# Kernel tuning notes

Measured on AMD Instinct MI355X. Metric: run time of the kernel, lower is better.

The kernel has to match this reference:

```python
import jax, jax.numpy as jnp
import numpy as np

D_MODEL = 1024
N_HEAD = 16
D_K = D_MODEL // N_HEAD
B, S = 4, 2048


def setup_inputs() -> dict:
    key = jax.random.key(0)
    ks = jax.random.split(key, 12)
    s = 1.0 / np.sqrt(D_MODEL)
    inp = {
        "q": jax.random.normal(ks[0], (B, S, D_MODEL), jnp.float32),
        "k": jax.random.normal(ks[1], (B, S, D_MODEL), jnp.float32),
        "v": jax.random.normal(ks[2], (B, S, D_MODEL), jnp.float32),
        "mask": jnp.tril(jnp.ones((S, S), dtype=bool)),
        "Wq": jax.random.normal(ks[3], (D_MODEL, D_MODEL), jnp.float32) * s,
        "bq": jnp.zeros((D_MODEL,), jnp.float32),
        "Wk": jax.random.normal(ks[4], (D_MODEL, D_MODEL), jnp.float32) * s,
        "bk": jnp.zeros((D_MODEL,), jnp.float32),
        "Wv": jax.random.normal(ks[5], (D_MODEL, D_MODEL), jnp.float32) * s,
        "bv": jnp.zeros((D_MODEL,), jnp.float32),
        "Wo": jax.random.normal(ks[6], (D_MODEL, D_MODEL), jnp.float32) * s,
        "bo": jnp.zeros((D_MODEL,), jnp.float32),
    }
    return inp


def reference(q, k, v, mask, Wq, bq, Wk, bk, Wv, bv, Wo, bo):
    b, n, d = q.shape
    # NOTE: source module (faithfully) computes the query projection from k.
    qh = (k @ Wq + bq).reshape(b, n, N_HEAD, D_K).transpose(0, 2, 1, 3)  # b h n d_k
    kh = (k @ Wk + bk).reshape(b, n, N_HEAD, D_K).transpose(0, 2, 1, 3)
    vh = (v @ Wv + bv).reshape(b, n, N_HEAD, D_K).transpose(0, 2, 1, 3)
    scores = jnp.einsum("bhqd,bhkd->bhqk", qh, kh) / jnp.sqrt(jnp.float32(D_K))
    scores = jnp.where(mask[None, None, :, :], scores, jnp.float32(-1e9))
    attn = jax.nn.softmax(scores, axis=-1)  # dropout is identity in eval
    out = jnp.einsum("bhqk,bhkd->bhqd", attn, vh)
    out = out.transpose(0, 2, 1, 3).reshape(b, n, d)
    out = out @ Wo + bo  # dropout identity in eval
    return out, attn
```

## Files before the change

kernel.cpp:

```cpp
#include <hip/hip_runtime.h>
#include <hip/hip_bf16.h>

#define S_LEN 2048
#define DMODEL 1024
#define NHEAD 16
#define DK 64
#define BS 4

typedef __attribute__((ext_vector_type(8))) short short8;
typedef __attribute__((ext_vector_type(4))) float f32x4;
typedef __attribute__((ext_vector_type(4))) ushort ushort4v;

__device__ __forceinline__ ushort f2b(float f) {
  __hip_bfloat16 h = __float2bfloat16(f);
  return __builtin_bit_cast(ushort, h);
}

__device__ __forceinline__ void gl_lds16(const void* g, void* l) {
  __builtin_amdgcn_global_load_lds(
      (const __attribute__((address_space(1))) void*)g,
      (__attribute__((address_space(3))) void*)l, 16, 0, 0);
}


__global__ __launch_bounds__(256) void cvt2_kernel(
    const float* __restrict__ a, const float* __restrict__ b,
    ushort* __restrict__ oa, ushort* __restrict__ ob, int n4) {
  int idx = blockIdx.x * 256 + threadIdx.x;
  int stride = gridDim.x * 256;
  for (int i = idx; i < 2 * n4; i += stride) {
    const bool first = (i < n4);
    const int j = first ? i : i - n4;
    f32x4 v = first ? ((const f32x4*)a)[j] : ((const f32x4*)b)[j];
    ushort4v o;
    o[0] = f2b(v[0]); o[1] = f2b(v[1]); o[2] = f2b(v[2]); o[3] = f2b(v[3]);
    if (first) ((ushort4v*)oa)[j] = o; else ((ushort4v*)ob)[j] = o;
  }
}

__global__ __launch_bounds__(256) void transW4_kernel(
    const float* __restrict__ W0, const float* __restrict__ W1,
    const float* __restrict__ W2, const float* __restrict__ W3,
    ushort* __restrict__ T0, ushort* __restrict__ T1,
    ushort* __restrict__ T2, ushort* __restrict__ T3) {
  const float* W;
  ushort* T;
  switch (blockIdx.z) {
    case 0: W = W0; T = T0; break;
    case 1: W = W1; T = T1; break;
    case 2: W = W2; T = T2; break;
    default: W = W3; T = T3; break;
  }
  __shared__ float t[32][33];
  const int n0 = blockIdx.x * 32, k0 = blockIdx.y * 32;
  const int tx = threadIdx.x, ty = threadIdx.y;
#pragma unroll
  for (int i = 0; i < 4; i++)
    t[ty + i * 8][tx] = W[(size_t)(k0 + ty + i * 8) * DMODEL + n0 + tx];
  __syncthreads();
#pragma unroll
  for (int i = 0; i < 4; i++)
    T[(size_t)(n0 + ty + i * 8) * DMODEL + k0 + tx] = f2b(t[tx][ty + i * 8]);
}

template <bool F32OUT, bool QKMODE, bool VT>
__global__ __launch_bounds__(256) void gemm_bt(
    const ushort* __restrict__ A, const ushort* __restrict__ Bt,
    const float* __restrict__ bias, const float* __restrict__ bias1,
    void* __restrict__ Cout, void* __restrict__ Cout1,
    int M, int N, int K) {
  __shared__ ushort Als[128 * 32];
  __shared__ ushort Bls[128 * 32];
  const int tid = threadIdx.x;
  const int lane = tid & 63;
  const int w = tid >> 6;
  const int lo = lane & 15, hi = lane >> 4;
  const int nb = N >> 7;
  const int bm = blockIdx.x / nb, bn = blockIdx.x % nb;
  const int m0 = bm << 7, n0 = bn << 7;
  const int wr = (w >> 1) << 6, wc = (w & 1) << 6;

  f32x4 acc[4][4] = {};

  const int c1 = tid, c2 = tid + 256;
  const int r1 = c1 >> 2, k1 = (c1 & 3) << 3;
  const int r2 = c2 >> 2, k2 = (c2 & 3) << 3;
  const ushort* Ap1 = A + (size_t)(m0 + r1) * K + k1;
  const ushort* Ap2 = A + (size_t)(m0 + r2) * K + k2;
  const ushort* Bp1 = Bt + (size_t)(n0 + r1) * K + k1;
  const ushort* Bp2 = Bt + (size_t)(n0 + r2) * K + k2;
  char* Al = (char*)Als;
  char* Bl = (char*)Bls;

  for (int k0 = 0; k0 < K; k0 += 32) {
    gl_lds16(Ap1 + k0, Al + c1 * 16);
    gl_lds16(Ap2 + k0, Al + c2 * 16);
    gl_lds16(Bp1 + k0, Bl + c1 * 16);
    gl_lds16(Bp2 + k0, Bl + c2 * 16);
    __syncthreads();
    short8 af[4], bf[4];
#pragma unroll
    for (int i = 0; i < 4; i++)
      af[i] = *(const short8*)(Als + (wr + i * 16 + lo) * 32 + hi * 8);
#pragma unroll
    for (int j = 0; j < 4; j++)
      bf[j] = *(const short8*)(Bls + (wc + j * 16 + lo) * 32 + hi * 8);
#pragma unroll
    for (int i = 0; i < 4; i++)
#pragma unroll
      for (int j = 0; j < 4; j++)
        acc[i][j] = __builtin_amdgcn_mfma_f32_16x16x32_bf16(af[i], bf[j], acc[i][j], 0, 0, 0);
    __syncthreads();
  }

#pragma unroll
  for (int j = 0; j < 4; j++) {
    const int col = n0 + wc + j * 16 + lo;
    const float* bp = (QKMODE && col >= 1024) ? bias1 : bias;
    const int colm = QKMODE ? (col & 1023) : col;
    const int cN = QKMODE ? 1024 : N;
    const float bj = bp ? bp[colm] : 0.0f;
    if (VT) {
#pragma unroll
      for (int i = 0; i < 4; i++) {
        const int row0 = m0 + wr + i * 16 + hi * 4;
        ushort4v pk;
#pragma unroll
        for (int r = 0; r < 4; r++) pk[r] = f2b(acc[i][j][r] + bj);
        *(ushort4v*)(&((ushort*)Cout)[(size_t)col * M + row0]) = pk;
      }
    } else {
#pragma unroll
      for (int i = 0; i < 4; i++) {
        const int row0 = m0 + wr + i * 16 + hi * 4;
#pragma unroll
        for (int r = 0; r < 4; r++) {
          float vv = acc[i][j][r] + bj;
          if (F32OUT) {
            __builtin_nontemporal_store(
                vv, &((float*)Cout)[(size_t)(row0 + r) * N + col]);
          } else {
            void* dst = (QKMODE && col >= 1024) ? Cout1 : Cout;
            ((ushort*)dst)[(size_t)(row0 + r) * cN + colm] = f2b(vv);
          }
        }
      }
    }
  }
}

#define SWZ(row) ((((row) & 7) << 5) ^ (((row) & 8) << 1))
__global__ __launch_bounds__(512) void attn_kernel(
    const ushort* __restrict__ Qh, const ushort* __restrict__ Kh,
    const ushort* __restrict__ Vt, float* __restrict__ attn,
    ushort* __restrict__ Ah) {
  const int blk = blockIdx.x;
  const int x = blk & 7;
  const int i2 = blk >> 3;
  const int g = x + ((i2 >> 4) << 3);
  const int tidx = i2 & 15;
  const int t = (tidx & 1) ? (tidx >> 1) : (15 - (tidx >> 1));
  const int h = g & 15;
  const int b = g >> 4;
  const int tid = threadIdx.x;
  const int w = tid >> 6;
  const int lane = tid & 63;
  const int lo = lane & 15, hi = lane >> 4;
  const int q0 = t << 7;
  const int qrow = w * 16 + lo;
  const int qg = q0 + qrow;
  const int tok0 = b * S_LEN + q0 + w * 16;
  const int ktmax = 2 * t + 1;
  const int ntiles = ktmax + 1;

  __shared__ ushort Kls[2][64 * 64];
  __shared__ ushort Vls[2][64 * 64];
  __shared__ float Pf[8][16 * 64];

  short8 aq[2];
  {
    const ushort* qp = Qh + (size_t)(tok0 + lo) * DMODEL + h * DK + hi * 8;
    aq[0] = *(const short8*)qp;
    aq[1] = *(const short8*)(qp + 32);
  }

  const ushort* kbh = Kh + (size_t)(b * S_LEN) * DMODEL + h * DK;
  const ushort* vbh = Vt + (size_t)(h * DK) * (BS * S_LEN) + b * S_LEN;

  const int srow = tid >> 3;
  const int scolb = ((tid & 7) << 4) ^ ((srow & 7) << 4);
  const ushort* ksrc = kbh + (size_t)srow * DMODEL + (scolb >> 1);
  const ushort* vsrc = vbh + (size_t)srow * (BS * S_LEN) + (scolb >> 1);

#define STAGE_K(buf, kt)                                                     \
  gl_lds16(ksrc + (size_t)(kt) * 64 * DMODEL, (char*)&Kls[(buf)][0] + tid * 16)
#define STAGE_V(buf, kt)                                                     \
  gl_lds16(vsrc + (size_t)(kt) * 64, (char*)&Vls[(buf)][0] + tid * 16)

#define QKT(sa, cur)                                                         \
  __builtin_amdgcn_s_setprio(1);                                             \
  _Pragma("unroll") for (int j = 0; j < 4; j++) {                            \
    const int row = j * 16 + lo;                                             \
    short8 b0 = *(const short8*)((const char*)&Kls[(cur)][0] + row * 128 +   \
                                 ((hi * 16) ^ ((row & 7) << 4)));            \
    sa[j] = __builtin_amdgcn_mfma_f32_16x16x32_bf16(b0, aq[0], sa[j], 0, 0, 0); \
  }                                                                          \
  _Pragma("unroll") for (int j = 0; j < 4; j++) {                            \
    const int row = j * 16 + lo;                                             \
    short8 b1 = *(const short8*)((const char*)&Kls[(cur)][0] + row * 128 +   \
                                 ((64 + hi * 16) ^ ((row & 7) << 4)));       \
    sa[j] = __builtin_amdgcn_mfma_f32_16x16x32_bf16(b1, aq[1], sa[j], 0, 0, 0); \
  }                                                                          \
  __builtin_amdgcn_s_setprio(0);

  float* abase =
      attn + (size_t)(b * NHEAD + h) * S_LEN * S_LEN + (size_t)q0 * S_LEN;

  const int zc0 = ntiles << 6;
  const int zcol = zc0 + tid * 4;
  const bool zon = (zcol < S_LEN);
  const f32x4 zv = {0.0f, 0.0f, 0.0f, 0.0f};

  float lsum = 0.0f;
  STAGE_K(0, 0);
  for (int kt = 0; kt <= ktmax; ++kt) {
    const int cur = kt & 1;
    __syncthreads();
    if (kt < ktmax) STAGE_K(cur ^ 1, kt + 1);
    if (zon) {
      const int r0 = (kt * 128) / ntiles;
      const int r1 = ((kt + 1) * 128) / ntiles;
      for (int row = r0; row < r1; ++row)
        __builtin_nontemporal_store(
            zv, (f32x4*)(abase + (size_t)row * S_LEN + zcol));
    }
    f32x4 sa[4] = {};
    QKT(sa, cur)
#pragma unroll
    for (int j = 0; j < 4; j++) {
#pragma unroll
      for (int r = 0; r < 4; r++) {
        const int kg = kt * 64 + j * 16 + hi * 4 + r;
        const float e = __expf(sa[j][r] * 0.125f);
        lsum += (kg > qg) ? 0.0f : e;
      }
    }
  }
  lsum += __shfl_xor(lsum, 16);
  lsum += __shfl_xor(lsum, 32);
  const float invl = 1.0f / lsum;

  f32x4 oacc[4] = {};

  __syncthreads();
  STAGE_K(0, 0);
  STAGE_V(0, 0);
  for (int kt = 0; kt <= ktmax; ++kt) {
    const int cur = kt & 1;
    __syncthreads();
    if (kt < ktmax) { STAGE_K(cur ^ 1, kt + 1); STAGE_V(cur ^ 1, kt + 1); }
    f32x4 sa[4] = {};
    QKT(sa, cur)
#pragma unroll
    for (int j = 0; j < 4; j++) {
      float p[4];
#pragma unroll
      for (int r = 0; r < 4; r++) {
        const int kg = kt * 64 + j * 16 + hi * 4 + r;
        p[r] = (kg > qg) ? 0.0f : __expf(sa[j][r] * 0.125f) * invl;
      }
      f32x4 pv4 = {p[0], p[1], p[2], p[3]};
      *(f32x4*)((char*)&Pf[w][0] + lo * 256 +
                ((j * 64 + hi * 16) ^ SWZ(lo))) = pv4;
    }
#pragma unroll
    for (int t2 = 0; t2 < 4; t2++) {
      const int rr = hi + 4 * t2;
      f32x4 pv = *(const f32x4*)((const char*)&Pf[w][0] + rr * 256 +
                                 ((lo * 16) ^ SWZ(rr)));
      __builtin_nontemporal_store(
          pv,
          (f32x4*)(abase + (size_t)(w * 16 + rr) * S_LEN + kt * 64 + lo * 4));
    }
    short8 ap[2];
#pragma unroll
    for (int ks = 0; ks < 2; ks++) {
      const int base = ks * 128 + hi * 32;
      f32x4 u0 = *(const f32x4*)((const char*)&Pf[w][0] + lo * 256 +
                                 ((base) ^ SWZ(lo)));
      f32x4 u1 = *(const f32x4*)((const char*)&Pf[w][0] + lo * 256 +
                                 ((base + 16) ^ SWZ(lo)));
      short8 a;
      a[0] = f2b(u0[0]); a[1] = f2b(u0[1]); a[2] = f2b(u0[2]); a[3] = f2b(u0[3]);
      a[4] = f2b(u1[0]); a[5] = f2b(u1[1]); a[6] = f2b(u1[2]); a[7] = f2b(u1[3]);
      ap[ks] = a;
    }
    __builtin_amdgcn_s_setprio(1);
#pragma unroll
    for (int dj = 0; dj < 4; dj++) {
      const int row = dj * 16 + lo;
      const char* vrow = (const char*)&Vls[cur][0] + row * 128;
      short8 b0 = *(const short8*)(vrow + ((hi * 16) ^ ((row & 7) << 4)));
      short8 b1 = *(const short8*)(vrow + ((64 + hi * 16) ^ ((row & 7) << 4)));
      oacc[dj] = __builtin_amdgcn_mfma_f32_16x16x32_bf16(ap[0], b0, oacc[dj], 0, 0, 0);
      oacc[dj] = __builtin_amdgcn_mfma_f32_16x16x32_bf16(ap[1], b1, oacc[dj], 0, 0, 0);
    }
    __builtin_amdgcn_s_setprio(0);
  }

#pragma unroll
  for (int dj = 0; dj < 4; dj++)
#pragma unroll
    for (int r = 0; r < 4; r++)
      Ah[(size_t)(tok0 + hi * 4 + r) * DMODEL + h * DK + dj * 16 + lo] =
          f2b(oacc[dj][r]);
#undef STAGE_K
#undef STAGE_V
#undef QKT
}


extern "C" void kernel_launch(void* const* d_in, const int* in_sizes, int n_in,
                              void* d_out, int out_size, void* d_ws,
                              size_t ws_size, hipStream_t stream) {
  const float* kin = (const float*)d_in[1];
  const float* vin = (const float*)d_in[2];
  const float* Wq = (const float*)d_in[4];
  const float* bq = (const float*)d_in[5];
  const float* Wk = (const float*)d_in[6];
  const float* bk = (const float*)d_in[7];
  const float* Wv = (const float*)d_in[8];
  const float* bv = (const float*)d_in[9];
  const float* Wo = (const float*)d_in[10];
  const float* bo = (const float*)d_in[11];

  float* out = (float*)d_out;
  float* attn = out + (size_t)BS * S_LEN * DMODEL;

  char* ws = (char*)d_ws;
  const size_t MB = (size_t)1 << 20;
  ushort* kb   = (ushort*)(ws + 0 * MB);
  ushort* vb   = (ushort*)(ws + 16 * MB);
  ushort* Qh   = (ushort*)(ws + 32 * MB);
  ushort* Kh   = (ushort*)(ws + 48 * MB);
  ushort* Vt   = (ushort*)(ws + 64 * MB);
  ushort* WqkT = (ushort*)(ws + 80 * MB);
  ushort* WvT  = (ushort*)(ws + 84 * MB);
  ushort* WoT  = (ushort*)(ws + 86 * MB);

  const int NTOK4 = (BS * S_LEN * DMODEL) / 4;
  cvt2_kernel<<<4096, 256, 0, stream>>>(kin, vin, kb, vb, NTOK4);

  dim3 tb(32, 8);
  transW4_kernel<<<dim3(32, 32, 4), tb, 0, stream>>>(
      Wq, Wk, Wv, Wo, WqkT, WqkT + (size_t)DMODEL * DMODEL, WvT, WoT);

  gemm_bt<false, true, false><<<64 * 16, 256, 0, stream>>>(
      kb, WqkT, bq, bk, Qh, Kh, 8192, 2048, 1024);
  gemm_bt<false, false, true><<<64 * 8, 256, 0, stream>>>(
      vb, WvT, bv, nullptr, Vt, nullptr, 8192, 1024, 1024);

  ushort* Ahp = kb;
  attn_kernel<<<BS * NHEAD * (S_LEN / 128), 512, 0, stream>>>(Qh, Kh, Vt, attn, Ahp);

  gemm_bt<true, false, false><<<64 * 8, 256, 0, stream>>>(
      Ahp, WoT, bo, nullptr, out, nullptr, 8192, 1024, 1024);
}
```

Baseline: 392.2 us.

## Move causal zero-fill of attention matrix into projection GEMMs and relax barriers

Zeroing of the fully-masked 128x128 upper-triangle tiles of the attention-probability output moves out of the attention kernel and into the Q/K and V projection GEMMs. Each GEMM block writes five such tiles, addressed by a triangular-index decode, once its main loop finishes. The goal is to run this large write stream alongside compute-bound GEMM work instead of inside the attention loop. The second attention pass also replaces its per-iteration __syncthreads with an explicit vmcnt wait plus barrier at the loop end, so prefetch loads can stay in flight. This relies on exact knowledge of outstanding load counts and on the float sqrt-based tile decode being correct.

```diff
diff --git a/kernel.cpp b/kernel.cpp
--- a/kernel.cpp
+++ b/kernel.cpp
@@ -63,12 +63,12 @@
     T[(size_t)(n0 + ty + i * 8) * DMODEL + k0 + tx] = f2b(t[tx][ty + i * 8]);
 }
 
-template <bool F32OUT, bool QKMODE, bool VT>
+template <bool F32OUT, bool QKMODE, bool VT, bool FILL>
 __global__ __launch_bounds__(256) void gemm_bt(
     const ushort* __restrict__ A, const ushort* __restrict__ Bt,
     const float* __restrict__ bias, const float* __restrict__ bias1,
     void* __restrict__ Cout, void* __restrict__ Cout1,
-    int M, int N, int K) {
+    int M, int N, int K, float* __restrict__ fillb, int slab0) {
   __shared__ ushort Als[128 * 32];
   __shared__ ushort Bls[128 * 32];
   const int tid = threadIdx.x;
@@ -111,6 +111,39 @@
       for (int j = 0; j < 4; j++)
         acc[i][j] = __builtin_amdgcn_mfma_f32_16x16x32_bf16(af[i], bf[j], acc[i][j], 0, 0, 0);
     __syncthreads();
+  }
+
+  if (FILL) {
+    const f32x4 zv = {0.0f, 0.0f, 0.0f, 0.0f};
+    const int s0 = slab0 + blockIdx.x * 5;
+    float *fb0, *fb1, *fb2, *fb3, *fb4;
+#define SLAB_BASE(fb, ss)                                                   \
+  {                                                                         \
+    const int s = (ss);                                                     \
+    const int bh = s / 120;                                                 \
+    const int u = s - bh * 120;                                             \
+    const int j = (int)((1.0f + sqrtf(1.0f + 8.0f * (float)u)) * 0.5f);     \
+    const int rb = u - ((j * (j - 1)) >> 1);                                \
+    fb = fillb + (size_t)bh * S_LEN * S_LEN + (size_t)(rb * 128) * S_LEN +  \
+         j * 128;                                                           \
+  }
+    SLAB_BASE(fb0, s0)
+    SLAB_BASE(fb1, s0 + 1)
+    SLAB_BASE(fb2, s0 + 2)
+    SLAB_BASE(fb3, s0 + 3)
+    SLAB_BASE(fb4, s0 + 4)
+#undef SLAB_BASE
+#pragma unroll
+    for (int sl = 0; sl < 5; sl++) {
+      float* bp = (sl == 0) ? fb0 : (sl == 1) ? fb1 : (sl == 2) ? fb2
+                  : (sl == 3) ? fb3 : fb4;
+#pragma unroll
+      for (int q = 0; q < 16; q++) {
+        const int u2 = tid + (q << 8);
+        __builtin_nontemporal_store(
+            zv, (f32x4*)(bp + (size_t)(u2 >> 5) * S_LEN + (u2 & 31) * 4));
+      }
+    }
   }
 
 #pragma unroll
@@ -171,7 +204,6 @@
   const int qg = q0 + qrow;
   const int tok0 = b * S_LEN + q0 + w * 16;
   const int ktmax = 2 * t + 1;
-  const int ntiles = ktmax + 1;
 
   __shared__ ushort Kls[2][64 * 64];
   __shared__ ushort Vls[2][64 * 64];
@@ -216,24 +248,12 @@
   float* abase =
       attn + (size_t)(b * NHEAD + h) * S_LEN * S_LEN + (size_t)q0 * S_LEN;
 
-  const int zc0 = ntiles << 6;
-  const int zcol = zc0 + tid * 4;
-  const bool zon = (zcol < S_LEN);
-  const f32x4 zv = {0.0f, 0.0f, 0.0f, 0.0f};
-
   float lsum = 0.0f;
   STAGE_K(0, 0);
   for (int kt = 0; kt <= ktmax; ++kt) {
     const int cur = kt & 1;
     __syncthreads();
     if (kt < ktmax) STAGE_K(cur ^ 1, kt + 1);
-    if (zon) {
-      const int r0 = (kt * 128) / ntiles;
-      const int r1 = ((kt + 1) * 128) / ntiles;
-      for (int row = r0; row < r1; ++row)
-        __builtin_nontemporal_store(
-            zv, (f32x4*)(abase + (size_t)row * S_LEN + zcol));
-    }
     f32x4 sa[4] = {};
     QKT(sa, cur)
 #pragma unroll
@@ -251,13 +271,11 @@
   const float invl = 1.0f / lsum;
 
   f32x4 oacc[4] = {};
-
-  __syncthreads();
   STAGE_K(0, 0);
   STAGE_V(0, 0);
+  asm volatile("s_waitcnt vmcnt(0)\n\ts_barrier" ::: "memory");
   for (int kt = 0; kt <= ktmax; ++kt) {
     const int cur = kt & 1;
-    __syncthreads();
     if (kt < ktmax) { STAGE_K(cur ^ 1, kt + 1); STAGE_V(cur ^ 1, kt + 1); }
     f32x4 sa[4] = {};
     QKT(sa, cur)
@@ -306,6 +324,7 @@
       oacc[dj] = __builtin_amdgcn_mfma_f32_16x16x32_bf16(ap[1], b1, oacc[dj], 0, 0, 0);
     }
     __builtin_amdgcn_s_setprio(0);
+    asm volatile("s_waitcnt vmcnt(4)\n\ts_barrier" ::: "memory");
   }
 
 #pragma unroll
@@ -355,14 +374,14 @@
   transW4_kernel<<<dim3(32, 32, 4), tb, 0, stream>>>(
       Wq, Wk, Wv, Wo, WqkT, WqkT + (size_t)DMODEL * DMODEL, WvT, WoT);
 
-  gemm_bt<false, true, false><<<64 * 16, 256, 0, stream>>>(
-      kb, WqkT, bq, bk, Qh, Kh, 8192, 2048, 1024);
-  gemm_bt<false, false, true><<<64 * 8, 256, 0, stream>>>(
-      vb, WvT, bv, nullptr, Vt, nullptr, 8192, 1024, 1024);
+  gemm_bt<false, true, false, true><<<64 * 16, 256, 0, stream>>>(
+      kb, WqkT, bq, bk, Qh, Kh, 8192, 2048, 1024, attn, 0);
+  gemm_bt<false, false, true, true><<<64 * 8, 256, 0, stream>>>(
+      vb, WvT, bv, nullptr, Vt, nullptr, 8192, 1024, 1024, attn, 5120);
 
   ushort* Ahp = kb;
   attn_kernel<<<BS * NHEAD * (S_LEN / 128), 512, 0, stream>>>(Qh, Kh, Vt, attn, Ahp);
 
-  gemm_bt<true, false, false><<<64 * 8, 256, 0, stream>>>(
-      Ahp, WoT, bo, nullptr, out, nullptr, 8192, 1024, 1024);
-}
+  gemm_bt<true, false, false, false><<<64 * 8, 256, 0, stream>>>(
+      Ahp, WoT, bo, nullptr, out, nullptr, 8192, 1024, 1024, nullptr, 0);
+}
```

Result: slower. 423.3 us (+7.9%).

## Fuse fp32-to-bf16 activation conversion into projection GEMM A-tile loads

Applied to the files above, without the earlier changes.

Removes the separate conversion kernel that turned k and v into bf16 buffers. The projection GEMMs now load fp32 A tiles straight into LDS with an XOR swizzle and convert to bf16 when building MFMA fragments. This drops a full read-plus-write pass over the activations. In exchange the GEMM reads twice the A bytes, doubles A-tile LDS, and repeats conversion work for each N-tile block (16 blocks for QK).

```diff
diff --git a/kernel.cpp b/kernel.cpp
--- a/kernel.cpp
+++ b/kernel.cpp
@@ -22,21 +22,6 @@
       (__attribute__((address_space(3))) void*)l, 16, 0, 0);
 }
 
-
-__global__ __launch_bounds__(256) void cvt2_kernel(
-    const float* __restrict__ a, const float* __restrict__ b,
-    ushort* __restrict__ oa, ushort* __restrict__ ob, int n4) {
-  int idx = blockIdx.x * 256 + threadIdx.x;
-  int stride = gridDim.x * 256;
-  for (int i = idx; i < 2 * n4; i += stride) {
-    const bool first = (i < n4);
-    const int j = first ? i : i - n4;
-    f32x4 v = first ? ((const f32x4*)a)[j] : ((const f32x4*)b)[j];
-    ushort4v o;
-    o[0] = f2b(v[0]); o[1] = f2b(v[1]); o[2] = f2b(v[2]); o[3] = f2b(v[3]);
-    if (first) ((ushort4v*)oa)[j] = o; else ((ushort4v*)ob)[j] = o;
-  }
-}
 
 __global__ __launch_bounds__(256) void transW4_kernel(
     const float* __restrict__ W0, const float* __restrict__ W1,
@@ -63,13 +48,13 @@
     T[(size_t)(n0 + ty + i * 8) * DMODEL + k0 + tx] = f2b(t[tx][ty + i * 8]);
 }
 
-template <bool F32OUT, bool QKMODE, bool VT>
+template <bool F32OUT, bool QKMODE, bool VT, bool AF32>
 __global__ __launch_bounds__(256) void gemm_bt(
-    const ushort* __restrict__ A, const ushort* __restrict__ Bt,
+    const void* __restrict__ A, const ushort* __restrict__ Bt,
     const float* __restrict__ bias, const float* __restrict__ bias1,
     void* __restrict__ Cout, void* __restrict__ Cout1,
     int M, int N, int K) {
-  __shared__ ushort Als[128 * 32];
+  __shared__ ushort Als[AF32 ? 8192 : 4096];
   __shared__ ushort Bls[128 * 32];
   const int tid = threadIdx.x;
   const int lane = tid & 63;
@@ -85,23 +70,47 @@
   const int c1 = tid, c2 = tid + 256;
   const int r1 = c1 >> 2, k1 = (c1 & 3) << 3;
   const int r2 = c2 >> 2, k2 = (c2 & 3) << 3;
-  const ushort* Ap1 = A + (size_t)(m0 + r1) * K + k1;
-  const ushort* Ap2 = A + (size_t)(m0 + r2) * K + k2;
+  const ushort* Ap1 = (const ushort*)A + (size_t)(m0 + r1) * K + k1;
+  const ushort* Ap2 = (const ushort*)A + (size_t)(m0 + r2) * K + k2;
+  const int arow = tid >> 3;
+  const int acolb = ((tid & 7) << 4) ^ ((arow & 7) << 4);
+  const float* Afp = (const float*)A + (size_t)(m0 + arow) * K + (acolb >> 2);
   const ushort* Bp1 = Bt + (size_t)(n0 + r1) * K + k1;
   const ushort* Bp2 = Bt + (size_t)(n0 + r2) * K + k2;
   char* Al = (char*)Als;
   char* Bl = (char*)Bls;
 
   for (int k0 = 0; k0 < K; k0 += 32) {
-    gl_lds16(Ap1 + k0, Al + c1 * 16);
-    gl_lds16(Ap2 + k0, Al + c2 * 16);
+    if (AF32) {
+      gl_lds16(Afp + k0, Al + tid * 16);
+      gl_lds16(Afp + (size_t)32 * K + k0, Al + (tid + 256) * 16);
+      gl_lds16(Afp + (size_t)64 * K + k0, Al + (tid + 512) * 16);
+      gl_lds16(Afp + (size_t)96 * K + k0, Al + (tid + 768) * 16);
+    } else {
+      gl_lds16(Ap1 + k0, Al + c1 * 16);
+      gl_lds16(Ap2 + k0, Al + c2 * 16);
+    }
     gl_lds16(Bp1 + k0, Bl + c1 * 16);
     gl_lds16(Bp2 + k0, Bl + c2 * 16);
     __syncthreads();
     short8 af[4], bf[4];
-#pragma unroll
-    for (int i = 0; i < 4; i++)
-      af[i] = *(const short8*)(Als + (wr + i * 16 + lo) * 32 + hi * 8);
+    if (AF32) {
+#pragma unroll
+      for (int i = 0; i < 4; i++) {
+        const int R = wr + i * 16 + lo;
+        const char* rb = Al + R * 128;
+        f32x4 u0 = *(const f32x4*)(rb + ((hi * 32) ^ ((R & 7) << 4)));
+        f32x4 u1 = *(const f32x4*)(rb + ((hi * 32 + 16) ^ ((R & 7) << 4)));
+        short8 a;
+        a[0] = f2b(u0[0]); a[1] = f2b(u0[1]); a[2] = f2b(u0[2]); a[3] = f2b(u0[3]);
+        a[4] = f2b(u1[0]); a[5] = f2b(u1[1]); a[6] = f2b(u1[2]); a[7] = f2b(u1[3]);
+        af[i] = a;
+      }
+    } else {
+#pragma unroll
+      for (int i = 0; i < 4; i++)
+        af[i] = *(const short8*)(Als + (wr + i * 16 + lo) * 32 + hi * 8);
+    }
 #pragma unroll
     for (int j = 0; j < 4; j++)
       bf[j] = *(const short8*)(Bls + (wc + j * 16 + lo) * 32 + hi * 8);
@@ -339,8 +348,7 @@
 
   char* ws = (char*)d_ws;
   const size_t MB = (size_t)1 << 20;
-  ushort* kb   = (ushort*)(ws + 0 * MB);
-  ushort* vb   = (ushort*)(ws + 16 * MB);
+  ushort* Ahp  = (ushort*)(ws + 0 * MB);
   ushort* Qh   = (ushort*)(ws + 32 * MB);
   ushort* Kh   = (ushort*)(ws + 48 * MB);
   ushort* Vt   = (ushort*)(ws + 64 * MB);
@@ -348,21 +356,17 @@
   ushort* WvT  = (ushort*)(ws + 84 * MB);
   ushort* WoT  = (ushort*)(ws + 86 * MB);
 
-  const int NTOK4 = (BS * S_LEN * DMODEL) / 4;
-  cvt2_kernel<<<4096, 256, 0, stream>>>(kin, vin, kb, vb, NTOK4);
-
   dim3 tb(32, 8);
   transW4_kernel<<<dim3(32, 32, 4), tb, 0, stream>>>(
       Wq, Wk, Wv, Wo, WqkT, WqkT + (size_t)DMODEL * DMODEL, WvT, WoT);
 
-  gemm_bt<false, true, false><<<64 * 16, 256, 0, stream>>>(
-      kb, WqkT, bq, bk, Qh, Kh, 8192, 2048, 1024);
-  gemm_bt<false, false, true><<<64 * 8, 256, 0, stream>>>(
-      vb, WvT, bv, nullptr, Vt, nullptr, 8192, 1024, 1024);
-
-  ushort* Ahp = kb;
+  gemm_bt<false, true, false, true><<<64 * 16, 256, 0, stream>>>(
+      kin, WqkT, bq, bk, Qh, Kh, 8192, 2048, 1024);
+  gemm_bt<false, false, true, true><<<64 * 8, 256, 0, stream>>>(
+      vin, WvT, bv, nullptr, Vt, nullptr, 8192, 1024, 1024);
+
   attn_kernel<<<BS * NHEAD * (S_LEN / 128), 512, 0, stream>>>(Qh, Kh, Vt, attn, Ahp);
 
-  gemm_bt<true, false, false><<<64 * 8, 256, 0, stream>>>(
+  gemm_bt<true, false, false, false><<<64 * 8, 256, 0, stream>>>(
       Ahp, WoT, bo, nullptr, out, nullptr, 8192, 1024, 1024);
 }
```

Measured after the change: 396.3 us. About the same (+1.0%).
